# Optimization experiments

Measured on AMD Instinct MI355X. Metric: run time of the kernel, lower is better.

Reference implementation:

```python
import jax, jax.numpy as jnp
import numpy as np

N_NODES = 20000
N_EDGES = 320000
D_IN = 256      # n_source_nodes (input feature dim)
HEADS = 4
HEAD_DIM = 64   # n_target_nodes // heads
D_OUT = HEADS * HEAD_DIM  # n_target_nodes = 256
EDGE_DIM = 1


def setup_inputs() -> dict:
    key = jax.random.key(0)
    ks = jax.random.split(key, 12)
    s = 0.05
    return {
        "x": jax.random.normal(ks[0], (N_NODES, D_IN), jnp.float32),
        "edge_index": jax.random.randint(ks[1], (2, N_EDGES), 0, N_NODES, jnp.int64),
        "edge_attr": jax.random.normal(ks[2], (N_EDGES, EDGE_DIM), jnp.float32),
        # TransformerConv params (weights stored [in, out]; PyG Linear defaults: q/k/v have bias, edge lin has no bias, skip lin has bias)
        "Wq": jax.random.normal(ks[3], (D_IN, D_OUT), jnp.float32) * s,
        "bq": jnp.zeros((D_OUT,), jnp.float32),
        "Wk": jax.random.normal(ks[4], (D_IN, D_OUT), jnp.float32) * s,
        "bk": jnp.zeros((D_OUT,), jnp.float32),
        "Wv": jax.random.normal(ks[5], (D_IN, D_OUT), jnp.float32) * s,
        "bv": jnp.zeros((D_OUT,), jnp.float32),
        "We": jax.random.normal(ks[6], (EDGE_DIM, D_OUT), jnp.float32) * s,
        "Wskip": jax.random.normal(ks[7], (D_IN, D_OUT), jnp.float32) * s,
        "bskip": jnp.zeros((D_OUT,), jnp.float32),
        # GraphNorm params
        "gn_weight": jnp.ones((D_OUT,), jnp.float32),
        "gn_bias": jnp.zeros((D_OUT,), jnp.float32),
        "gn_mean_scale": jnp.ones((D_OUT,), jnp.float32),
    }


def reference(x, edge_index, edge_attr, Wq, bq, Wk, bk, Wv, bv, We, Wskip, bskip, gn_weight, gn_bias, gn_mean_scale):
    N = x.shape[0]
    src, dst = edge_index[0], edge_index[1]  # message flows src -> dst (source_to_target)

    q = (x @ Wq + bq).reshape(N, HEADS, HEAD_DIM)
    k = (x @ Wk + bk).reshape(N, HEADS, HEAD_DIM)
    v = (x @ Wv + bv).reshape(N, HEADS, HEAD_DIM)
    e = (edge_attr @ We).reshape(-1, HEADS, HEAD_DIM)  # [E, H, C]

    k_j = k[src] + e                                   # [E, H, C]
    alpha = jnp.einsum('ehc,ehc->eh', q[dst], k_j) / jnp.sqrt(jnp.float32(HEAD_DIM))

    # segment softmax over edges sharing the same target node
    a_max = jax.ops.segment_max(alpha, dst, num_segments=N)[dst]
    a_exp = jnp.exp(alpha - a_max)
    a_sum = jax.ops.segment_sum(a_exp, dst, num_segments=N)[dst]
    att = a_exp / (a_sum + 1e-16)                      # [E, H]

    msg = (v[src] + e) * att[..., None]                # [E, H, C]
    out = jax.ops.segment_sum(msg, dst, num_segments=N).reshape(N, D_OUT)
    out = out + x @ Wskip + bskip                      # root/skip connection (beta=False)

    # GraphNorm (single graph): weight*(x - alpha*mean)/sqrt(var+eps) + bias
    mean = out.mean(axis=0)
    centered = out - gn_mean_scale * mean
    var = jnp.mean(centered * centered, axis=0)
    out = gn_weight * centered * jax.lax.rsqrt(var + 1e-5) + gn_bias

    out = jax.nn.relu(out)
    xt = out.T @ out                                   # [D_OUT, D_OUT]
    xt_min, xt_max = jnp.min(xt), jnp.max(xt)
    return (xt - xt_min) / (xt_max - xt_min + 1e-8)
```

## Files before the change

kernel.cpp:

```cpp
#include <hip/hip_runtime.h>
#include <math.h>

#define N_NODES 20000
#define N_EDGES 320000
#define SK 20480
#define APAD 80
#define GPITCH 144

typedef short short8 __attribute__((ext_vector_type(8)));
typedef float f32x4 __attribute__((ext_vector_type(4)));

static __device__ __forceinline__ unsigned short f2bf(float f) {
    unsigned int u = __float_as_uint(f);
    u = (u + 0x7FFF + ((u >> 16) & 1)) >> 16;
    return (unsigned short)u;
}
static __device__ __forceinline__ float b2f(unsigned short u) {
    return __uint_as_float((unsigned int)u << 16);
}
static __device__ __forceinline__ float blo(unsigned int u) {
    return __uint_as_float(u << 16);
}
static __device__ __forceinline__ float bhi(unsigned int u) {
    return __uint_as_float(u & 0xFFFF0000u);
}

__global__ __launch_bounds__(256) void prep_k(const float* __restrict__ x,
                                              unsigned short* __restrict__ xb,
                                              const float* __restrict__ Wq,
                                              const float* __restrict__ Wk,
                                              const float* __restrict__ Wv,
                                              const float* __restrict__ Wsk,
                                              const float* __restrict__ bq,
                                              const float* __restrict__ bk,
                                              const float* __restrict__ bv,
                                              const float* __restrict__ bsk,
                                              unsigned short* __restrict__ wT,
                                              float* __restrict__ bias_all,
                                              const int* __restrict__ dst,
                                              int* __restrict__ deg)
{
    const int b = blockIdx.x;
    const int tid = threadIdx.x;
    if (b < 2500) {
        const size_t base = ((size_t)b * 256 + tid) * 8;
        const float4 f0 = *(const float4*)(x + base);
        const float4 f1 = *(const float4*)(x + base + 4);
        ushort4 u0, u1;
        u0.x = f2bf(f0.x); u0.y = f2bf(f0.y); u0.z = f2bf(f0.z); u0.w = f2bf(f0.w);
        u1.x = f2bf(f1.x); u1.y = f2bf(f1.y); u1.z = f2bf(f1.z); u1.w = f2bf(f1.w);
        *(ushort4*)(xb + base) = u0;
        *(ushort4*)(xb + base + 4) = u1;
    } else if (b < 3524) {
        const int bb = b - 2500;
        const int wi = bb >> 8, n = bb & 255;
        const float* W = (wi == 0) ? Wq : (wi == 1) ? Wk : (wi == 2) ? Wv : Wsk;
        wT[(size_t)bb * 256 + tid] = f2bf(W[(size_t)tid * 256 + n]);
        if (tid == 0) {
            const float* bv_ = (wi == 0) ? bq : (wi == 1) ? bk : (wi == 2) ? bv : bsk;
            bias_all[bb] = bv_[n];
        }
    } else {
        const int e = (b - 3524) * 256 + tid;
        if (e < N_EDGES) atomicAdd(&deg[dst[e]], 1);
    }
}

__global__ __launch_bounds__(256, 4) void gemm_qkvs(const unsigned short* __restrict__ xb,
                                                    const unsigned short* __restrict__ wT,
                                                    const float* __restrict__ bias_all,
                                                    unsigned short* __restrict__ qb,
                                                    unsigned short* __restrict__ kvb,
                                                    unsigned short* __restrict__ ob)
{
    __shared__ __align__(16) unsigned short As[(128 + 128) * APAD];
    unsigned short* Bs = As + 128 * APAD;
    float* stage = (float*)As;

    const int tid  = threadIdx.x;
    const int lane = tid & 63;
    const int w    = tid >> 6;
    const int wm = w >> 1, wn = w & 1;
    const int row0 = blockIdx.x * 128;
    const int by   = blockIdx.y;
    const int wsel = by >> 1;
    const int ar = tid >> 1, ak = (tid & 1) * 32;
    const int fr = lane & 15, fk = (lane >> 4) * 8, lg = lane >> 4;

    int gr = row0 + ar; gr = gr < N_NODES ? gr : N_NODES - 1;
    const unsigned short* ab = xb + (size_t)gr * 256 + ak;
    const unsigned short* bb = wT + (size_t)(by * 128 + ar) * 256 + ak;

    f32x4 acc[4][4] = {};
    uint4 a0, a1, a2, a3, b0, b1, b2, b3;

    a0 = *(const uint4*)ab;        a1 = *(const uint4*)(ab + 8);
    a2 = *(const uint4*)(ab + 16); a3 = *(const uint4*)(ab + 24);
    b0 = *(const uint4*)bb;        b1 = *(const uint4*)(bb + 8);
    b2 = *(const uint4*)(bb + 16); b3 = *(const uint4*)(bb + 24);

#pragma unroll
    for (int it = 0; it < 4; ++it) {
        __syncthreads();
        unsigned short* asp = &As[ar * APAD + ak];
        *(uint4*)asp        = a0;
        *(uint4*)(asp + 8)  = a1;
        *(uint4*)(asp + 16) = a2;
        *(uint4*)(asp + 24) = a3;
        unsigned short* bsp = &Bs[ar * APAD + ak];
        *(uint4*)bsp        = b0;
        *(uint4*)(bsp + 8)  = b1;
        *(uint4*)(bsp + 16) = b2;
        *(uint4*)(bsp + 24) = b3;
        __syncthreads();
        if (it < 3) {
            const unsigned short* ap = ab + (it + 1) * 64;
            const unsigned short* bp = bb + (it + 1) * 64;
            a0 = *(const uint4*)ap;        a1 = *(const uint4*)(ap + 8);
            a2 = *(const uint4*)(ap + 16); a3 = *(const uint4*)(ap + 24);
            b0 = *(const uint4*)bp;        b1 = *(const uint4*)(bp + 8);
            b2 = *(const uint4*)(bp + 16); b3 = *(const uint4*)(bp + 24);
        }
#pragma unroll
        for (int ks = 0; ks < 2; ++ks) {
            short8 af[4], bf[4];
#pragma unroll
            for (int m = 0; m < 4; ++m)
                af[m] = *(const short8*)&As[(wm * 64 + m * 16 + fr) * APAD + ks * 32 + fk];
#pragma unroll
            for (int n = 0; n < 4; ++n)
                bf[n] = *(const short8*)&Bs[(wn * 64 + n * 16 + fr) * APAD + ks * 32 + fk];
#pragma unroll
            for (int m = 0; m < 4; ++m)
#pragma unroll
                for (int n = 0; n < 4; ++n)
                    acc[m][n] = __builtin_amdgcn_mfma_f32_16x16x32_bf16(af[m], bf[n], acc[m][n], 0, 0, 0);
        }
    }
    __syncthreads();

    float badd[4];
#pragma unroll
    for (int n = 0; n < 4; ++n) badd[n] = bias_all[by * 128 + wn * 64 + n * 16 + fr];

    float* st = stage + w * 1024;
    const int chalf = by & 1;
#pragma unroll
    for (int m = 0; m < 4; ++m) {
#pragma unroll
        for (int n = 0; n < 4; ++n)
#pragma unroll
            for (int r = 0; r < 4; ++r)
                st[(lg * 4 + r) * 64 + n * 16 + fr] = acc[m][n][r] + badd[n];
#pragma unroll
        for (int it = 0; it < 4; ++it) {
            const int lrow = it * 4 + lg;
            const f32x4 c4 = *(const f32x4*)&st[lrow * 64 + fr * 4];
            const int grow = row0 + wm * 64 + m * 16 + lrow;
            if (grow < N_NODES) {
                const int colin = chalf * 128 + wn * 64 + fr * 4;
                ushort4 u;
                u.x = f2bf(c4[0]); u.y = f2bf(c4[1]); u.z = f2bf(c4[2]); u.w = f2bf(c4[3]);
                if (wsel == 3) {
                    *(ushort4*)(ob + (size_t)grow * 256 + colin) = u;
                } else if (wsel == 0) {
                    *(ushort4*)(qb + (size_t)grow * 256 + colin) = u;
                } else {
                    const int c = chalf * 32 + wn * 16 + fr;
                    const size_t kvidx = (size_t)grow * 512 + c * 8 + (wsel == 1 ? 0 : 4);
                    *(ushort4*)(kvb + kvidx) = u;
                }
            }
        }
    }
}

__global__ __launch_bounds__(1024) void scan_k(const int* __restrict__ deg,
                                               int* __restrict__ row_start)
{
    __shared__ int sdeg[20480];
    const int tid = threadIdx.x;
    const int lane = tid & 63, wid = tid >> 6;
    const int CH = 20;
#pragma unroll
    for (int i = 0; i < 20; ++i) {
        const int idx = i * 1024 + tid;
        sdeg[idx] = (idx < N_NODES) ? deg[idx] : 0;
    }
    __syncthreads();
    const int base = tid * CH;
    int local[CH];
    int s = 0;
#pragma unroll
    for (int i = 0; i < CH; ++i) {
        local[i] = s;
        s += sdeg[base + i];
    }
    int v = s;
#pragma unroll
    for (int off = 1; off < 64; off <<= 1) {
        const int t = __shfl_up(v, off);
        if (lane >= off) v += t;
    }
    __shared__ int wsum[16];
    if (lane == 63) wsum[wid] = v;
    __syncthreads();
    if (tid == 0) {
        int r = 0;
        for (int i = 0; i < 16; ++i) { const int t = wsum[i]; wsum[i] = r; r += t; }
    }
    __syncthreads();
    const int excl = v - s + wsum[wid];
#pragma unroll
    for (int i = 0; i < CH; ++i) {
        const int idx = base + i;
        if (idx < N_NODES) row_start[idx] = excl + local[i];
    }
    if (tid == 1023) row_start[N_NODES] = excl + s;
}

__global__ void fill_csr(const int* __restrict__ dst, const int* __restrict__ src,
                         const float* __restrict__ ea,
                         const int* __restrict__ row_start,
                         int* __restrict__ cursor, int2* __restrict__ ekv)
{
    const int e = blockIdx.x * 256 + threadIdx.x;
    if (e < N_EDGES) {
        const int d = dst[e];
        const int p = atomicAdd(&cursor[d], 1);
        int2 pk;
        pk.x = src[e];
        pk.y = __float_as_int(ea[e]);
        ekv[row_start[d] + p] = pk;
    }
}

static __device__ __forceinline__ void edge_step(const uint4 kv, const float a,
                                                 const float4 qf, const float4 we4,
                                                 float& ssum, float& ax, float& ay,
                                                 float& az, float& aw)
{
    const float k0 = blo(kv.x), k1 = bhi(kv.x), k2 = blo(kv.y), k3 = bhi(kv.y);
    const float v0 = blo(kv.z), v1 = bhi(kv.z), v2 = blo(kv.w), v3 = bhi(kv.w);
    float p = qf.x * (k0 + a * we4.x) + qf.y * (k1 + a * we4.y)
            + qf.z * (k2 + a * we4.z) + qf.w * (k3 + a * we4.w);
    p += __shfl_xor(p, 1); p += __shfl_xor(p, 2);
    p += __shfl_xor(p, 4); p += __shfl_xor(p, 8);
    const float wgt = __expf(p * 0.125f);
    ssum += wgt;
    ax += wgt * (v0 + a * we4.x);
    ay += wgt * (v1 + a * we4.y);
    az += wgt * (v2 + a * we4.z);
    aw += wgt * (v3 + a * we4.w);
}

__global__ __launch_bounds__(256) void attn_k(const unsigned short* __restrict__ qb,
                                              const unsigned short* __restrict__ kvb,
                                              const float* __restrict__ We,
                                              const int* __restrict__ row_start,
                                              const int2* __restrict__ ekv,
                                              unsigned short* __restrict__ out)
{
    const int wid  = threadIdx.x >> 6;
    const int lane = threadIdx.x & 63;
    const int n = blockIdx.x * 4 + wid;

    const ushort4 qv = *(const ushort4*)(qb + (size_t)n * 256 + lane * 4);
    float4 qf;
    qf.x = b2f(qv.x); qf.y = b2f(qv.y); qf.z = b2f(qv.z); qf.w = b2f(qv.w);
    const float4 we4 = *(const float4*)(We + lane * 4);
    const int rs = row_start[n], re = row_start[n + 1];
    const int lo8 = lane * 8;

    float ssum = 0.f;
    float ax = 0.f, ay = 0.f, az = 0.f, aw = 0.f;

    int s = rs;
    for (; s + 4 <= re; s += 4) {
        const int2 p0 = ekv[s],     p1 = ekv[s + 1];
        const int2 p2 = ekv[s + 2], p3 = ekv[s + 3];
        const uint4 kv0 = *(const uint4*)(kvb + (size_t)p0.x * 512 + lo8);
        const uint4 kv1 = *(const uint4*)(kvb + (size_t)p1.x * 512 + lo8);
        const uint4 kv2 = *(const uint4*)(kvb + (size_t)p2.x * 512 + lo8);
        const uint4 kv3 = *(const uint4*)(kvb + (size_t)p3.x * 512 + lo8);
        edge_step(kv0, __int_as_float(p0.y), qf, we4, ssum, ax, ay, az, aw);
        edge_step(kv1, __int_as_float(p1.y), qf, we4, ssum, ax, ay, az, aw);
        edge_step(kv2, __int_as_float(p2.y), qf, we4, ssum, ax, ay, az, aw);
        edge_step(kv3, __int_as_float(p3.y), qf, we4, ssum, ax, ay, az, aw);
    }
    for (; s < re; ++s) {
        const int2 p0 = ekv[s];
        const uint4 kv0 = *(const uint4*)(kvb + (size_t)p0.x * 512 + lo8);
        edge_step(kv0, __int_as_float(p0.y), qf, we4, ssum, ax, ay, az, aw);
    }
    const float inv = 1.f / (ssum + 1e-16f);
    const ushort4 sk4 = *(const ushort4*)(out + (size_t)n * 256 + lane * 4);
    ushort4 ou;
    ou.x = f2bf(ax * inv + b2f(sk4.x));
    ou.y = f2bf(ay * inv + b2f(sk4.y));
    ou.z = f2bf(az * inv + b2f(sk4.z));
    ou.w = f2bf(aw * inv + b2f(sk4.w));
    *(ushort4*)(out + (size_t)n * 256 + lane * 4) = ou;
}

__global__ __launch_bounds__(256) void gn_stats_k(const unsigned short* __restrict__ out,
                                                  float* __restrict__ gstats)
{
    const int c = threadIdx.x;
    float s = 0.f, s2 = 0.f;
    for (int r = blockIdx.x; r < N_NODES; r += gridDim.x) {
        const float vv = b2f(out[(size_t)r * 256 + c]);
        s += vv; s2 += vv * vv;
    }
    atomicAdd(&gstats[c], s);
    atomicAdd(&gstats[256 + c], s2);
}

__global__ __launch_bounds__(256) void norm_relu_T(const unsigned short* __restrict__ ob,
                                                   const float* __restrict__ gstats,
                                                   const float* __restrict__ gw,
                                                   const float* __restrict__ gb,
                                                   const float* __restrict__ gms,
                                                   unsigned short* __restrict__ obT)
{
    __shared__ unsigned short tile[256][72];
    __shared__ float smu[256], swi[256], sbd[256];
    const int t = threadIdx.x;
    const int r0 = blockIdx.x * 64;
    {
        const float invN = 1.f / (float)N_NODES;
        const float mean = gstats[t] * invN;
        const float exx  = gstats[256 + t] * invN;
        const float mu   = gms[t] * mean;
        const float var  = exx - 2.f * mu * mean + mu * mu;
        smu[t] = mu;
        swi[t] = gw[t] * rsqrtf(var + 1e-5f);
        sbd[t] = gb[t];
    }
    __syncthreads();
    const int rr = t >> 2;
    const int row = r0 + rr;
#pragma unroll
    for (int it = 0; it < 16; ++it) {
        const int col = it * 16 + (t & 3) * 4;
        ushort4 u;
        if (row < N_NODES) {
            const ushort4 uv = *(const ushort4*)(ob + (size_t)row * 256 + col);
            u.x = f2bf(fmaxf((b2f(uv.x) - smu[col + 0]) * swi[col + 0] + sbd[col + 0], 0.f));
            u.y = f2bf(fmaxf((b2f(uv.y) - smu[col + 1]) * swi[col + 1] + sbd[col + 1], 0.f));
            u.z = f2bf(fmaxf((b2f(uv.z) - smu[col + 2]) * swi[col + 2] + sbd[col + 2], 0.f));
            u.w = f2bf(fmaxf((b2f(uv.w) - smu[col + 3]) * swi[col + 3] + sbd[col + 3], 0.f));
        } else { u.x = u.y = u.z = u.w = 0; }
        tile[col + 0][rr] = u.x;
        tile[col + 1][rr] = u.y;
        tile[col + 2][rr] = u.z;
        tile[col + 3][rr] = u.w;
    }
    __syncthreads();
#pragma unroll
    for (int it = 0; it < 8; ++it) {
        const int c = it * 32 + (t >> 3);
        const int part = t & 7;
        const uint4 x0 = *(const uint4*)&tile[c][part * 8];
        *(uint4*)(obT + (size_t)c * SK + r0 + part * 8) = x0;
    }
}

__global__ __launch_bounds__(256) void gram_k(const unsigned short* __restrict__ obT,
                                              float* __restrict__ xt)
{
    const int bi_l[10] = {0,0,0,0,1,1,1,2,2,3};
    const int bj_l[10] = {0,1,2,3,1,2,3,2,3,3};
    const int bi = bi_l[blockIdx.x], bj = bj_l[blockIdx.x];
    const int r0 = blockIdx.y * 512;

    __shared__ __align__(16) unsigned short Ai[64 * GPITCH];
    __shared__ __align__(16) unsigned short Aj[64 * GPITCH];
    const int tid = threadIdx.x;
    const int lane = tid & 63;
    const int w = tid >> 6;
    const int wi = w >> 1, wj = w & 1;
    const int lr = tid >> 2, kseg = (tid & 3) * 32;
    const int fr = lane & 15, fk = (lane >> 4) * 8, lg = lane >> 4;

    f32x4 acc[2][2] = {};

    for (int kt = 0; kt < 512; kt += 128) {
        uint4 ai[4], aj[4];
        const unsigned short* pa = obT + (size_t)(bi * 64 + lr) * SK + r0 + kt + kseg;
        const unsigned short* pb = obT + (size_t)(bj * 64 + lr) * SK + r0 + kt + kseg;
#pragma unroll
        for (int j = 0; j < 4; ++j) { ai[j] = *(const uint4*)(pa + 8 * j); aj[j] = *(const uint4*)(pb + 8 * j); }
        __syncthreads();
#pragma unroll
        for (int j = 0; j < 4; ++j) {
            *(uint4*)&Ai[lr * GPITCH + kseg + 8 * j] = ai[j];
            *(uint4*)&Aj[lr * GPITCH + kseg + 8 * j] = aj[j];
        }
        __syncthreads();
#pragma unroll
        for (int ks = 0; ks < 4; ++ks) {
            short8 af[2], bf[2];
#pragma unroll
            for (int m = 0; m < 2; ++m)
                af[m] = *(const short8*)&Ai[(wi * 32 + m * 16 + fr) * GPITCH + ks * 32 + fk];
#pragma unroll
            for (int n = 0; n < 2; ++n)
                bf[n] = *(const short8*)&Aj[(wj * 32 + n * 16 + fr) * GPITCH + ks * 32 + fk];
#pragma unroll
            for (int m = 0; m < 2; ++m)
#pragma unroll
                for (int n = 0; n < 2; ++n)
                    acc[m][n] = __builtin_amdgcn_mfma_f32_16x16x32_bf16(af[m], bf[n], acc[m][n], 0, 0, 0);
        }
    }
#pragma unroll
    for (int m = 0; m < 2; ++m)
#pragma unroll
        for (int n = 0; n < 2; ++n)
#pragma unroll
            for (int r = 0; r < 4; ++r)
                atomicAdd(&xt[(size_t)(bi * 64 + wi * 32 + m * 16 + lg * 4 + r) * 256
                              + bj * 64 + wj * 32 + n * 16 + fr], acc[m][n][r]);
}

__global__ __launch_bounds__(1024) void minmax_fin_k(const float* __restrict__ xt,
                                                     float* __restrict__ outp)
{
    const int tid = threadIdx.x;
    float mn = 1e30f, mx = -1e30f;
    for (int i = tid; i < 65536; i += 1024) {
        const int r = i >> 8, c = i & 255;
        if ((r >> 6) <= (c >> 6)) {
            const float v = xt[i];
            mn = fminf(mn, v);
            mx = fmaxf(mx, v);
        }
    }
    for (int off = 1; off < 64; off <<= 1) {
        mn = fminf(mn, __shfl_xor(mn, off));
        mx = fmaxf(mx, __shfl_xor(mx, off));
    }
    __shared__ float smn[16], smx[16];
    __shared__ float fmn, fmx;
    const int w = tid >> 6;
    if ((tid & 63) == 0) { smn[w] = mn; smx[w] = mx; }
    __syncthreads();
    if (tid == 0) {
        for (int i = 1; i < 16; ++i) {
            mn = fminf(mn, smn[i]);
            mx = fmaxf(mx, smx[i]);
        }
        fmn = mn; fmx = mx;
    }
    __syncthreads();
    const float gmn = fmn;
    const float inv = 1.f / (fmx - gmn + 1e-8f);
    for (int i = tid; i < 65536; i += 1024) {
        const int r = i >> 8, c = i & 255;
        const float v = ((r >> 6) <= (c >> 6)) ? xt[i] : xt[c * 256 + r];
        outp[i] = (v - gmn) * inv;
    }
}

extern "C" void kernel_launch(void* const* d_in, const int* in_sizes, int n_in,
                              void* d_out, int out_size, void* d_ws, size_t ws_size,
                              hipStream_t stream)
{
    (void)in_sizes; (void)n_in; (void)out_size; (void)ws_size;
    const float* x   = (const float*)d_in[0];
    const int*   ei  = (const int*)d_in[1];
    const float* ea  = (const float*)d_in[2];
    const float* Wq  = (const float*)d_in[3];
    const float* bq  = (const float*)d_in[4];
    const float* Wk  = (const float*)d_in[5];
    const float* bk  = (const float*)d_in[6];
    const float* Wv  = (const float*)d_in[7];
    const float* bv  = (const float*)d_in[8];
    const float* We  = (const float*)d_in[9];
    const float* Wsk = (const float*)d_in[10];
    const float* bsk = (const float*)d_in[11];
    const float* gw  = (const float*)d_in[12];
    const float* gb  = (const float*)d_in[13];
    const float* gms = (const float*)d_in[14];
    float* outp = (float*)d_out;

    char* ws = (char*)d_ws;
    size_t off = 0;
    #define WS_ALLOC(nbytes) (ws + off); off = (off + (size_t)(nbytes) + 255) & ~(size_t)255
    unsigned short* xb  = (unsigned short*)WS_ALLOC((size_t)N_NODES * 256 * 2);
    unsigned short* wT  = (unsigned short*)WS_ALLOC((size_t)1024 * 256 * 2);
    float* bias_all     = (float*)WS_ALLOC(1024 * 4);
    unsigned short* qb  = (unsigned short*)WS_ALLOC((size_t)N_NODES * 256 * 2);
    unsigned short* kvb = (unsigned short*)WS_ALLOC((size_t)N_NODES * 512 * 2);
    unsigned short* ob  = (unsigned short*)WS_ALLOC((size_t)N_NODES * 256 * 2);
    const size_t zoff = off;
    int*   deg    = (int*)WS_ALLOC((size_t)N_NODES * 4);
    int*   cur    = (int*)WS_ALLOC((size_t)N_NODES * 4);
    float* gstats = (float*)WS_ALLOC(512 * 4);
    float* xt     = (float*)WS_ALLOC(65536 * 4);
    const size_t zbytes = off - zoff;
    int* row_start = (int*)WS_ALLOC((size_t)(N_NODES + 1) * 4);
    #undef WS_ALLOC
    int2* ekv           = (int2*)xb;
    unsigned short* obT = (unsigned short*)xb;

    const int* srcv = ei;
    const int* dstv = ei + N_EDGES;

    hipMemsetAsync(ws + zoff, 0, zbytes, stream);

    prep_k<<<2500 + 1024 + 1250, 256, 0, stream>>>(x, xb, Wq, Wk, Wv, Wsk,
                                                   bq, bk, bv, bsk, wT, bias_all,
                                                   dstv, deg);

    gemm_qkvs<<<dim3((N_NODES + 127) / 128, 8), 256, 0, stream>>>(xb, wT, bias_all,
                                                                  qb, kvb, ob);

    scan_k<<<1, 1024, 0, stream>>>(deg, row_start);
    fill_csr<<<(N_EDGES + 255) / 256, 256, 0, stream>>>(dstv, srcv, ea, row_start, cur, ekv);

    attn_k<<<N_NODES / 4, 256, 0, stream>>>(qb, kvb, We, row_start, ekv, ob);

    gn_stats_k<<<400, 256, 0, stream>>>(ob, gstats);
    norm_relu_T<<<320, 256, 0, stream>>>(ob, gstats, gw, gb, gms, obT);

    gram_k<<<dim3(10, 40), 256, 0, stream>>>(obT, xt);
    minmax_fin_k<<<1, 1024, 0, stream>>>(xt, outp);
}
```

Before: 227.1 us.

## Store K in fp8 with split K/V layout; double-buffer gram kernel over more blocks

K projections are now stored as packed fp8 and V stays bf16, in a new per-node row layout (K block, then V block). This cuts the bytes gathered per edge in the attention kernel from 16 to 12 per lane. Separately, the gram kernel halves its K-range per block, doubles the grid, and prefetches the second tile while computing the first. Using fp8 for K lowers the precision of the attention scores, which risks accuracy drift.

```diff
diff --git a/kernel.cpp b/kernel.cpp
--- a/kernel.cpp
+++ b/kernel.cpp
@@ -6,9 +6,11 @@
 #define SK 20480
 #define APAD 80
 #define GPITCH 144
+#define KVROW 768
 
 typedef short short8 __attribute__((ext_vector_type(8)));
 typedef float f32x4 __attribute__((ext_vector_type(4)));
+typedef float f32x2 __attribute__((ext_vector_type(2)));
 
 static __device__ __forceinline__ unsigned short f2bf(float f) {
     unsigned int u = __float_as_uint(f);
@@ -17,12 +19,6 @@
 }
 static __device__ __forceinline__ float b2f(unsigned short u) {
     return __uint_as_float((unsigned int)u << 16);
-}
-static __device__ __forceinline__ float blo(unsigned int u) {
-    return __uint_as_float(u << 16);
-}
-static __device__ __forceinline__ float bhi(unsigned int u) {
-    return __uint_as_float(u & 0xFFFF0000u);
 }
 
 __global__ __launch_bounds__(256) void prep_k(const float* __restrict__ x,
@@ -70,7 +66,7 @@
                                                     const unsigned short* __restrict__ wT,
                                                     const float* __restrict__ bias_all,
                                                     unsigned short* __restrict__ qb,
-                                                    unsigned short* __restrict__ kvb,
+                                                    unsigned char* __restrict__ kvb,
                                                     unsigned short* __restrict__ ob)
 {
     __shared__ __align__(16) unsigned short As[(128 + 128) * APAD];
@@ -159,16 +155,20 @@
             const int grow = row0 + wm * 64 + m * 16 + lrow;
             if (grow < N_NODES) {
                 const int colin = chalf * 128 + wn * 64 + fr * 4;
-                ushort4 u;
-                u.x = f2bf(c4[0]); u.y = f2bf(c4[1]); u.z = f2bf(c4[2]); u.w = f2bf(c4[3]);
-                if (wsel == 3) {
-                    *(ushort4*)(ob + (size_t)grow * 256 + colin) = u;
-                } else if (wsel == 0) {
-                    *(ushort4*)(qb + (size_t)grow * 256 + colin) = u;
+                if (wsel == 1) {
+                    int pk = __builtin_amdgcn_cvt_pk_fp8_f32(c4[0], c4[1], 0, false);
+                    pk = __builtin_amdgcn_cvt_pk_fp8_f32(c4[2], c4[3], pk, true);
+                    *(unsigned int*)(kvb + (size_t)grow * KVROW + colin) = (unsigned int)pk;
                 } else {
-                    const int c = chalf * 32 + wn * 16 + fr;
-                    const size_t kvidx = (size_t)grow * 512 + c * 8 + (wsel == 1 ? 0 : 4);
-                    *(ushort4*)(kvb + kvidx) = u;
+                    ushort4 u;
+                    u.x = f2bf(c4[0]); u.y = f2bf(c4[1]); u.z = f2bf(c4[2]); u.w = f2bf(c4[3]);
+                    if (wsel == 3) {
+                        *(ushort4*)(ob + (size_t)grow * 256 + colin) = u;
+                    } else if (wsel == 0) {
+                        *(ushort4*)(qb + (size_t)grow * 256 + colin) = u;
+                    } else {
+                        *(ushort4*)(kvb + (size_t)grow * KVROW + 256 + colin * 2) = u;
+                    }
                 }
             }
         }
@@ -235,27 +235,28 @@
     }
 }
 
-static __device__ __forceinline__ void edge_step(const uint4 kv, const float a,
+static __device__ __forceinline__ void edge_step(const unsigned int ku, const ushort4 vv,
+                                                 const float a,
                                                  const float4 qf, const float4 we4,
                                                  float& ssum, float& ax, float& ay,
                                                  float& az, float& aw)
 {
-    const float k0 = blo(kv.x), k1 = bhi(kv.x), k2 = blo(kv.y), k3 = bhi(kv.y);
-    const float v0 = blo(kv.z), v1 = bhi(kv.z), v2 = blo(kv.w), v3 = bhi(kv.w);
-    float p = qf.x * (k0 + a * we4.x) + qf.y * (k1 + a * we4.y)
-            + qf.z * (k2 + a * we4.z) + qf.w * (k3 + a * we4.w);
+    const f32x2 k01 = __builtin_amdgcn_cvt_pk_f32_fp8((int)ku, false);
+    const f32x2 k23 = __builtin_amdgcn_cvt_pk_f32_fp8((int)ku, true);
+    float p = qf.x * (k01[0] + a * we4.x) + qf.y * (k01[1] + a * we4.y)
+            + qf.z * (k23[0] + a * we4.z) + qf.w * (k23[1] + a * we4.w);
     p += __shfl_xor(p, 1); p += __shfl_xor(p, 2);
     p += __shfl_xor(p, 4); p += __shfl_xor(p, 8);
     const float wgt = __expf(p * 0.125f);
     ssum += wgt;
-    ax += wgt * (v0 + a * we4.x);
-    ay += wgt * (v1 + a * we4.y);
-    az += wgt * (v2 + a * we4.z);
-    aw += wgt * (v3 + a * we4.w);
+    ax += wgt * (b2f(vv.x) + a * we4.x);
+    ay += wgt * (b2f(vv.y) + a * we4.y);
+    az += wgt * (b2f(vv.z) + a * we4.z);
+    aw += wgt * (b2f(vv.w) + a * we4.w);
 }
 
 __global__ __launch_bounds__(256) void attn_k(const unsigned short* __restrict__ qb,
-                                              const unsigned short* __restrict__ kvb,
+                                              const unsigned char* __restrict__ kvb,
                                               const float* __restrict__ We,
                                               const int* __restrict__ row_start,
                                               const int2* __restrict__ ekv,
@@ -270,7 +271,8 @@
     qf.x = b2f(qv.x); qf.y = b2f(qv.y); qf.z = b2f(qv.z); qf.w = b2f(qv.w);
     const float4 we4 = *(const float4*)(We + lane * 4);
     const int rs = row_start[n], re = row_start[n + 1];
-    const int lo8 = lane * 8;
+    const int koff = lane << 2;
+    const int voff = 256 + (lane << 3);
 
     float ssum = 0.f;
     float ax = 0.f, ay = 0.f, az = 0.f, aw = 0.f;
@@ -279,19 +281,29 @@
     for (; s + 4 <= re; s += 4) {
         const int2 p0 = ekv[s],     p1 = ekv[s + 1];
         const int2 p2 = ekv[s + 2], p3 = ekv[s + 3];
-        const uint4 kv0 = *(const uint4*)(kvb + (size_t)p0.x * 512 + lo8);
-        const uint4 kv1 = *(const uint4*)(kvb + (size_t)p1.x * 512 + lo8);
-        const uint4 kv2 = *(const uint4*)(kvb + (size_t)p2.x * 512 + lo8);
-        const uint4 kv3 = *(const uint4*)(kvb + (size_t)p3.x * 512 + lo8);
-        edge_step(kv0, __int_as_float(p0.y), qf, we4, ssum, ax, ay, az, aw);
-        edge_step(kv1, __int_as_float(p1.y), qf, we4, ssum, ax, ay, az, aw);
-        edge_step(kv2, __int_as_float(p2.y), qf, we4, ssum, ax, ay, az, aw);
-        edge_step(kv3, __int_as_float(p3.y), qf, we4, ssum, ax, ay, az, aw);
+        const unsigned char* r0p = kvb + (size_t)p0.x * KVROW;
+        const unsigned char* r1p = kvb + (size_t)p1.x * KVROW;
+        const unsigned char* r2p = kvb + (size_t)p2.x * KVROW;
+        const unsigned char* r3p = kvb + (size_t)p3.x * KVROW;
+        const unsigned int k0 = *(const unsigned int*)(r0p + koff);
+        const ushort4      v0 = *(const ushort4*)(r0p + voff);
+        const unsigned int k1 = *(const unsigned int*)(r1p + koff);
+        const ushort4      v1 = *(const ushort4*)(r1p + voff);
+        const unsigned int k2 = *(const unsigned int*)(r2p + koff);
+        const ushort4      v2 = *(const ushort4*)(r2p + voff);
+        const unsigned int k3 = *(const unsigned int*)(r3p + koff);
+        const ushort4      v3 = *(const ushort4*)(r3p + voff);
+        edge_step(k0, v0, __int_as_float(p0.y), qf, we4, ssum, ax, ay, az, aw);
+        edge_step(k1, v1, __int_as_float(p1.y), qf, we4, ssum, ax, ay, az, aw);
+        edge_step(k2, v2, __int_as_float(p2.y), qf, we4, ssum, ax, ay, az, aw);
+        edge_step(k3, v3, __int_as_float(p3.y), qf, we4, ssum, ax, ay, az, aw);
     }
     for (; s < re; ++s) {
         const int2 p0 = ekv[s];
-        const uint4 kv0 = *(const uint4*)(kvb + (size_t)p0.x * 512 + lo8);
-        edge_step(kv0, __int_as_float(p0.y), qf, we4, ssum, ax, ay, az, aw);
+        const unsigned char* r0p = kvb + (size_t)p0.x * KVROW;
+        const unsigned int k0 = *(const unsigned int*)(r0p + koff);
+        const ushort4      v0 = *(const ushort4*)(r0p + voff);
+        edge_step(k0, v0, __int_as_float(p0.y), qf, we4, ssum, ax, ay, az, aw);
     }
     const float inv = 1.f / (ssum + 1e-16f);
     const ushort4 sk4 = *(const ushort4*)(out + (size_t)n * 256 + lane * 4);
@@ -372,7 +384,7 @@
     const int bi_l[10] = {0,0,0,0,1,1,1,2,2,3};
     const int bj_l[10] = {0,1,2,3,1,2,3,2,3,3};
     const int bi = bi_l[blockIdx.x], bj = bj_l[blockIdx.x];
-    const int r0 = blockIdx.y * 512;
+    const int r0 = blockIdx.y * 256;
 
     __shared__ __align__(16) unsigned short Ai[64 * GPITCH];
     __shared__ __align__(16) unsigned short Aj[64 * GPITCH];
@@ -385,12 +397,14 @@
 
     f32x4 acc[2][2] = {};
 
-    for (int kt = 0; kt < 512; kt += 128) {
-        uint4 ai[4], aj[4];
-        const unsigned short* pa = obT + (size_t)(bi * 64 + lr) * SK + r0 + kt + kseg;
-        const unsigned short* pb = obT + (size_t)(bj * 64 + lr) * SK + r0 + kt + kseg;
-#pragma unroll
-        for (int j = 0; j < 4; ++j) { ai[j] = *(const uint4*)(pa + 8 * j); aj[j] = *(const uint4*)(pb + 8 * j); }
+    const unsigned short* pa = obT + (size_t)(bi * 64 + lr) * SK + r0 + kseg;
+    const unsigned short* pb = obT + (size_t)(bj * 64 + lr) * SK + r0 + kseg;
+    uint4 ai[4], aj[4];
+#pragma unroll
+    for (int j = 0; j < 4; ++j) { ai[j] = *(const uint4*)(pa + 8 * j); aj[j] = *(const uint4*)(pb + 8 * j); }
+
+#pragma unroll
+    for (int itr = 0; itr < 2; ++itr) {
         __syncthreads();
 #pragma unroll
         for (int j = 0; j < 4; ++j) {
@@ -398,6 +412,13 @@
             *(uint4*)&Aj[lr * GPITCH + kseg + 8 * j] = aj[j];
         }
         __syncthreads();
+        if (itr == 0) {
+#pragma unroll
+            for (int j = 0; j < 4; ++j) {
+                ai[j] = *(const uint4*)(pa + 128 + 8 * j);
+                aj[j] = *(const uint4*)(pb + 128 + 8 * j);
+            }
+        }
 #pragma unroll
         for (int ks = 0; ks < 4; ++ks) {
             short8 af[2], bf[2];
@@ -492,7 +513,7 @@
     unsigned short* wT  = (unsigned short*)WS_ALLOC((size_t)1024 * 256 * 2);
     float* bias_all     = (float*)WS_ALLOC(1024 * 4);
     unsigned short* qb  = (unsigned short*)WS_ALLOC((size_t)N_NODES * 256 * 2);
-    unsigned short* kvb = (unsigned short*)WS_ALLOC((size_t)N_NODES * 512 * 2);
+    unsigned char*  kvb = (unsigned char*)WS_ALLOC((size_t)N_NODES * KVROW);
     unsigned short* ob  = (unsigned short*)WS_ALLOC((size_t)N_NODES * 256 * 2);
     const size_t zoff = off;
     int*   deg    = (int*)WS_ALLOC((size_t)N_NODES * 4);
@@ -525,6 +546,6 @@
     gn_stats_k<<<400, 256, 0, stream>>>(ob, gstats);
     norm_relu_T<<<320, 256, 0, stream>>>(ob, gstats, gw, gb, gms, obT);
 
-    gram_k<<<dim3(10, 40), 256, 0, stream>>>(obT, xt);
+    gram_k<<<dim3(10, 80), 256, 0, stream>>>(obT, xt);
     minmax_fin_k<<<1, 1024, 0, stream>>>(xt, outp);
 }
```

Result: faster. 218.9 us (-3.6%).
